# Kernel optimization log

Hardware: AMD Instinct MI355X
Metric: run time of the kernel (lower is better)

Reference implementation:

```python
import jax, jax.numpy as jnp
import numpy as np

S, M, B, D, H, DH = 1024, 1024, 4, 1024, 16, 64
T = S + M
EPS = 1e-5


def setup_inputs() -> dict:
    key = jax.random.key(0)
    ks = jax.random.split(key, 6)
    x = jax.random.normal(ks[0], (S, B, D), dtype=jnp.float32)
    pos_emb = jax.random.normal(ks[1], (S, 1, D), dtype=jnp.float32)
    memory = jax.random.normal(ks[2], (M, B, D), dtype=jnp.float32)
    # causal mask: query i (global position M+i) cannot attend to key j > M+i
    i = jnp.arange(S)[:, None]
    j = jnp.arange(T)[None, :]
    mask = jnp.broadcast_to((j > (i + M))[:, :, None], (S, T, B))  # [S,T,B] bool
    w_qkv = jax.random.normal(ks[3], (D, 3 * H * DH), dtype=jnp.float32) * (D ** -0.5)
    w_o = jax.random.normal(ks[4], (H * DH, D), dtype=jnp.float32) * ((H * DH) ** -0.5)
    ln_gamma = jnp.ones((D,), dtype=jnp.float32)
    ln_beta = jnp.zeros((D,), dtype=jnp.float32)
    return {"x": x, "pos_emb": pos_emb, "memory": memory, "mask": mask,
            "w_qkv": w_qkv, "w_o": w_o, "ln_gamma": ln_gamma, "ln_beta": ln_beta}


def reference(x, pos_emb, memory, mask, w_qkv, w_o, ln_gamma, ln_beta):
    seq_len = x.shape[0]
    scale = 1.0 / (DH ** 0.5)
    x = x + pos_emb[-seq_len:]                      # [S,B,D]
    c = jnp.concatenate([memory, x], axis=0)        # [T,B,D]
    qkv = jnp.einsum('tbd,de->tbe', c, w_qkv)       # [T,B,3*H*DH]
    q, k, v = jnp.split(qkv, 3, axis=-1)
    q = q.reshape(-1, B, H, DH)[-seq_len:]          # [S,B,H,DH]
    k = k.reshape(-1, B, H, DH)                     # [T,B,H,DH]
    v = v.reshape(-1, B, H, DH)
    score = jnp.einsum('ibnd,jbnd->ijbn', q, k) * scale  # [S,T,B,H]
    score = jnp.where(mask[:, :, :, None], -jnp.inf, score)
    prob = jax.nn.softmax(score, axis=1)
    vec = jnp.einsum('ijbn,jbnd->ibnd', prob, v)    # [S,B,H,DH]
    vec = vec.reshape(seq_len, B, H * DH)
    attn_out = jnp.einsum('sbe,ed->sbd', vec, w_o)  # [S,B,D]
    y = x + attn_out
    mu = jnp.mean(y, axis=-1, keepdims=True)
    var = jnp.mean(jnp.square(y - mu), axis=-1, keepdims=True)
    out = (y - mu) * jax.lax.rsqrt(var + EPS) * ln_gamma + ln_beta
    return out
```

## Files before the change

### kernel.cpp

```cpp
#include <hip/hip_runtime.h>
#include <stdint.h>

#define S_  1024
#define M_  1024
#define B_  4
#define D_  1024
#define H_  16
#define DH_ 64
#define T_  2048

typedef __attribute__((ext_vector_type(8))) short bf8;
typedef __attribute__((ext_vector_type(4))) float f32x4;
typedef __attribute__((ext_vector_type(16))) float f32x16;
typedef __attribute__((ext_vector_type(8))) unsigned short u16x8;
typedef __attribute__((ext_vector_type(4))) unsigned short u16x4;
typedef __attribute__((ext_vector_type(4))) unsigned int u32x4;
typedef unsigned short u16;

#define MFMA(a, b, c)   __builtin_amdgcn_mfma_f32_16x16x32_bf16((a), (b), (c), 0, 0, 0)
#define MFMA32(a, b, c) __builtin_amdgcn_mfma_f32_32x32x16_bf16((a), (b), (c), 0, 0, 0)

#define SIG(r) ((((r) >> 1) ^ ((r) >> 3)) & 3)

static __device__ __forceinline__ u16 f2bf(float f) {
  unsigned int u = __builtin_bit_cast(unsigned int, f);
  u += 0x7fffu + ((u >> 16) & 1u);
  return (u16)(u >> 16);
}

static __device__ __forceinline__ void gload16(const void* g, void* l) {
  __builtin_amdgcn_global_load_lds((const __attribute__((address_space(1))) unsigned int*)g,
                                   (__attribute__((address_space(3))) unsigned int*)l,
                                   16, 0, 0);
}

static __device__ __forceinline__ float fexp2(float x) {
  return __builtin_amdgcn_exp2f(x);
}
static __device__ __forceinline__ unsigned int cvtpk(float lo, float hi) {
  unsigned int r; asm("v_cvt_pk_bf16_f32 %0, %1, %2" : "=v"(r) : "v"(lo), "v"(hi)); return r;
}
static __device__ __forceinline__ void plswap(unsigned int& a, unsigned int& b) {
  asm volatile("s_nop 1\n\tv_permlane32_swap_b32 %0, %1" : "+v"(a), "+v"(b));
}

__global__ __launch_bounds__(256) void k_prep(const float* __restrict__ x,
    const float* __restrict__ pos, const float* __restrict__ mem,
    u16* __restrict__ cbf, float* __restrict__ xp)
{
  const int gid = blockIdx.x * 256 + threadIdx.x;
  const int e = gid * 8;
  const int row = e >> 10, col = e & 1023;
  float4 v0, v1;
  if (e < M_ * B_ * D_) {
    v0 = *(const float4*)(mem + e);
    v1 = *(const float4*)(mem + e + 4);
  } else {
    const int i2 = e - M_ * B_ * D_;
    v0 = *(const float4*)(x + i2);
    v1 = *(const float4*)(x + i2 + 4);
    const int srow = i2 >> 12;
    const float4 p0 = *(const float4*)(pos + srow * 1024 + col);
    const float4 p1 = *(const float4*)(pos + srow * 1024 + col + 4);
    v0.x += p0.x; v0.y += p0.y; v0.z += p0.z; v0.w += p0.w;
    v1.x += p1.x; v1.y += p1.y; v1.z += p1.z; v1.w += p1.w;
    *(float4*)(xp + i2) = v0;
    *(float4*)(xp + i2 + 4) = v1;
  }
  u16x8 c;
  c[0] = f2bf(v0.x); c[1] = f2bf(v0.y); c[2] = f2bf(v0.z); c[3] = f2bf(v0.w);
  c[4] = f2bf(v1.x); c[5] = f2bf(v1.y); c[6] = f2bf(v1.z); c[7] = f2bf(v1.w);
  const int ch = col >> 3;
  const int chs = (ch & ~3) | ((ch & 3) ^ SIG(row));
  *(u16x8*)(cbf + (size_t)row * 1024 + chs * 8) = c;
}

__global__ __launch_bounds__(256) void k_wtrans2(const float* __restrict__ wqkv,
    const float* __restrict__ wo, u16* __restrict__ wqt, u16* __restrict__ wot)
{
  __shared__ float tl[64][65];
  const int by = blockIdx.y;
  const float* src; u16* dst; int Cc, swz, c0;
  if (by < 48) { src = wqkv; dst = wqt; Cc = 3072; swz = 1; c0 = by * 64; }
  else         { src = wo;   dst = wot; Cc = 1024; swz = 0; c0 = (by - 48) * 64; }
  const int Rr = 1024;
  const int r0 = blockIdx.x * 64;
  const int tid = threadIdx.x;
  const int lr = tid >> 4, lc = (tid & 15) * 4;
  for (int i = 0; i < 4; ++i) {
    const int rr = lr + i * 16;
    const float4 v = *(const float4*)(src + (size_t)(r0 + rr) * Cc + c0 + lc);
    tl[rr][lc] = v.x; tl[rr][lc + 1] = v.y; tl[rr][lc + 2] = v.z; tl[rr][lc + 3] = v.w;
  }
  __syncthreads();
  const int c = tid >> 2, k0 = (tid & 3) * 16;
  u16x8 a, b;
  for (int j = 0; j < 8; ++j) { a[j] = f2bf(tl[k0 + j][c]); b[j] = f2bf(tl[k0 + 8 + j][c]); }
  const int roww = c0 + c;
  int ch0 = (r0 + k0) >> 3, ch1 = ((r0 + k0) >> 3) + 1;
  if (swz) {
    const int sx = SIG(roww);
    ch0 = (ch0 & ~3) | ((ch0 & 3) ^ sx);
    ch1 = (ch1 & ~3) | ((ch1 & 3) ^ sx);
  }
  u16* dp = dst + (size_t)roww * Rr;
  *(u16x8*)(dp + ch0 * 8) = a;
  *(u16x8*)(dp + ch1 * 8) = b;
}

__global__ __launch_bounds__(256, 3) void k_gemm_qkvs(const u16* __restrict__ A,
    const u16* __restrict__ Bt, u16* __restrict__ Qd, u16* __restrict__ Kd,
    u16* __restrict__ VTd)
{
  __shared__ u16 sA[3][4096];
  __shared__ u16 sB[3][4096];
  const int tid = threadIdx.x, lane = tid & 63, wave = tid >> 6;
  const int lrow = lane & 15, lgrp = lane >> 4;
  const int wm = (wave >> 1) * 64, wn = (wave & 1) * 64;
  const int sr = lane >> 2, sk = (lane & 3) * 8;

  const int bid = blockIdx.x;
  const int lid = (bid & 7) * 160 + (bid >> 3);
  int rowb, colb;
  if (lid < 512) { rowb = lid >> 4; colb = 8 + (lid & 15); }
  else { const int l2 = lid - 512; const int q = l2 / 24; rowb = 32 + q; colb = l2 - q * 24; }
  const int row0 = rowb * 128, col0 = colb * 128;

  f32x4 acc[4][4];
#pragma unroll
  for (int i = 0; i < 4; ++i)
#pragma unroll
    for (int j = 0; j < 4; ++j) acc[i][j] = f32x4{0.f, 0.f, 0.f, 0.f};

#define STAGE_S(bufi, kt) do { const int k0_ = (kt) * 32;                      \
    _Pragma("unroll") for (int s_ = 0; s_ < 2; ++s_) {                         \
      const int rr_ = (wave * 2 + s_) * 16 + sr;                               \
      gload16(A + (size_t)(row0 + rr_) * 1024 + k0_ + sk,                      \
              &sA[bufi][(wave * 2 + s_) * 512]);                               \
      gload16(Bt + (size_t)(col0 + rr_) * 1024 + k0_ + sk,                     \
              &sB[bufi][(wave * 2 + s_) * 512]);                               \
    } } while (0)

  STAGE_S(0, 0); STAGE_S(1, 1);

  int c0 = 0;
#pragma unroll 1
  for (int t = 0; t < 32; ++t) {
    if (t < 31) { asm volatile("s_waitcnt vmcnt(4)" ::: "memory"); }
    else        { asm volatile("s_waitcnt vmcnt(0)" ::: "memory"); }
    __builtin_amdgcn_s_barrier();
    __builtin_amdgcn_sched_barrier(0);
    const int c2 = (c0 + 2 >= 3) ? c0 - 1 : c0 + 2;
    if (t <= 29) STAGE_S(c2, t + 2);
    bf8 af[4], bfv[4];
#pragma unroll
    for (int i = 0; i < 4; ++i) {
      const int r_ = wm + i * 16 + lrow;
      af[i] = *(const bf8*)&sA[c0][r_ * 32 + ((lgrp ^ SIG(r_)) << 3)];
    }
#pragma unroll
    for (int j = 0; j < 4; ++j) {
      const int r_ = wn + j * 16 + lrow;
      bfv[j] = *(const bf8*)&sB[c0][r_ * 32 + ((lgrp ^ SIG(r_)) << 3)];
    }
    __builtin_amdgcn_s_setprio(1);
#pragma unroll
    for (int i = 0; i < 4; ++i)
#pragma unroll
      for (int j = 0; j < 4; ++j) acc[i][j] = MFMA(af[i], bfv[j], acc[i][j]);
    __builtin_amdgcn_s_setprio(0);
    c0 = (c0 == 2) ? 0 : c0 + 1;
  }

  const int which = col0 >> 10;
#pragma unroll
  for (int i = 0; i < 4; ++i)
#pragma unroll
    for (int j = 0; j < 4; ++j)
#pragma unroll
      for (int r = 0; r < 4; ++r) {
        const int grow = row0 + wm + i * 16 + lgrp * 4 + r;
        const int gcol = col0 + wn + j * 16 + lrow;
        const u16 bv = f2bf(acc[i][j][r]);
        const int t = grow >> 2, bb2 = grow & 3;
        const int rem = gcol & 1023;
        const int bh = bb2 * 16 + (rem >> 6), dh = rem & 63;
        if (which == 0) {
          if (t >= M_) Qd[((size_t)bh * S_ + (t - M_)) * 64 + dh] = bv;
        } else if (which == 1) {
          Kd[((size_t)bh * T_ + t) * 64 + (dh ^ ((t & 7) << 3))] = bv;
        } else {
          VTd[((size_t)bh * 64 + dh) * T_ + (t & ~63) + ((t & 63) ^ ((dh & 7) << 3))] = bv;
        }
      }
}

__global__ __launch_bounds__(256) void k_gemm_out(const u16* __restrict__ A,
    const u16* __restrict__ Bt, const float* __restrict__ xp,
    float* __restrict__ y)
{
  __shared__ u16 sA[3][2048];
  __shared__ u16 sB[3][4096];
  const int tid = threadIdx.x, lane = tid & 63, wave = tid >> 6;
  const int lrow = lane & 15, lgrp = lane >> 4;
  const int wm = (wave >> 1) * 32, wn = (wave & 1) * 64;
  const int row0 = blockIdx.y * 64, col0 = blockIdx.x * 128;
  const int sr = lane >> 2, sk = (lane & 3) * 8;

  f32x4 acc[2][4];
  for (int i = 0; i < 2; ++i)
    for (int j = 0; j < 4; ++j) acc[i][j] = f32x4{0.f, 0.f, 0.f, 0.f};

#define STAGE_O(bufi, kt) do { const int k0_ = (kt) * 32;                      \
    const int rra_ = wave * 16 + sr;                                           \
    gload16(A + (size_t)(row0 + rra_) * 1024 + k0_ + sk,                       \
            &sA[bufi][wave * 512]);                                            \
    _Pragma("unroll") for (int s_ = 0; s_ < 2; ++s_) {                         \
      const int rrb_ = (wave * 2 + s_) * 16 + sr;                              \
      gload16(Bt + (size_t)(col0 + rrb_) * 1024 + k0_ + sk,                    \
              &sB[bufi][(wave * 2 + s_) * 512]);                               \
    } } while (0)

  STAGE_O(0, 0); STAGE_O(1, 1);

  int c0 = 0;
#pragma unroll 1
  for (int kt = 0; kt < 32; ++kt) {
    if (kt < 31) { asm volatile("s_waitcnt vmcnt(3)" ::: "memory"); }
    else         { asm volatile("s_waitcnt vmcnt(0)" ::: "memory"); }
    __builtin_amdgcn_s_barrier();
    __builtin_amdgcn_sched_barrier(0);
    const int c2 = (c0 + 2 >= 3) ? c0 - 1 : c0 + 2;
    if (kt <= 29) STAGE_O(c2, kt + 2);
    bf8 af[2], bfv[4];
    const u16* pa = &sA[c0][(wm + lrow) * 32 + lgrp * 8];
    const u16* pb = &sB[c0][(wn + lrow) * 32 + lgrp * 8];
#pragma unroll
    for (int i = 0; i < 2; ++i) af[i] = *(const bf8*)(pa + i * 512);
#pragma unroll
    for (int j = 0; j < 4; ++j) bfv[j] = *(const bf8*)(pb + j * 512);
    __builtin_amdgcn_s_setprio(1);
#pragma unroll
    for (int i = 0; i < 2; ++i)
#pragma unroll
      for (int j = 0; j < 4; ++j) acc[i][j] = MFMA(af[i], bfv[j], acc[i][j]);
    __builtin_amdgcn_s_setprio(0);
    c0 = (c0 == 2) ? 0 : c0 + 1;
  }

  for (int i = 0; i < 2; ++i)
    for (int j = 0; j < 4; ++j)
      for (int r = 0; r < 4; ++r) {
        const int grow = row0 + wm + i * 16 + lgrp * 4 + r;
        const int gcol = col0 + wn + j * 16 + lrow;
        y[(size_t)grow * 1024 + gcol] = acc[i][j][r] + xp[(size_t)grow * 1024 + gcol];
      }
}

__global__ __launch_bounds__(256) void k_attn(const u16* __restrict__ Qd,
    const u16* __restrict__ Kd, const u16* __restrict__ VTd,
    u16* __restrict__ vec)
{
  __shared__ u16 Kl[2][4096];
  __shared__ u16 Vl[2][4096];
  const int tid = threadIdx.x, lane = tid & 63, wave = tid >> 6;
  const int ql = lane & 31, hi = lane >> 5;
  const int bid = blockIdx.x;
  const int sw = (bid & 7) * 64 + (bid >> 3);
  const int bh = sw >> 3, qb = sw & 7;
  const int bb = bh >> 4, hh = bh & 15;
  const int q0 = qb * 128 + wave * 32;
  const int myq = q0 + ql;
  const int klim = M_ + myq;

  bf8 qf[4];
  const u16* qrow = Qd + ((size_t)bh * S_ + myq) * 64 + hi * 8;
#pragma unroll
  for (int c = 0; c < 4; ++c) qf[c] = *(const bf8*)(qrow + c * 16);

  const u16* kb = Kd + (size_t)bh * T_ * 64;
  const u16* vb = VTd + (size_t)bh * 64 * T_;

  f32x16 o0, o1;
#pragma unroll
  for (int r = 0; r < 16; ++r) { o0[r] = 0.f; o1[r] = 0.f; }
  float m_run = 0.f, l_run = 0.f;
  const float cs = 0.125f * 1.44269504f;

  const int nkt = (M_ + qb * 128 + 128) >> 6;

  auto stage = [&](int buf, int kt) {
    const int t0 = kt * 64;
#pragma unroll
    for (int i = 0; i < 2; ++i) {
      const int ch = i * 256 + tid;
      gload16(kb + (size_t)t0 * 64 + ch * 8, &Kl[buf][ch * 8]);
    }
#pragma unroll
    for (int i = 0; i < 2; ++i) {
      const int ch = i * 256 + tid;
      gload16(vb + (size_t)(ch >> 3) * T_ + t0 + (ch & 7) * 8, &Vl[buf][ch * 8]);
    }
  };

  stage(0, 0);
  int cur = 0;
  for (int kt = 0; kt < nkt; ++kt) {
    if (kt + 1 < nkt) {
      stage(cur ^ 1, kt + 1);
      asm volatile("s_waitcnt vmcnt(4)" ::: "memory");
    } else {
      asm volatile("s_waitcnt vmcnt(0)" ::: "memory");
    }
    __builtin_amdgcn_s_barrier();

    const u16* Kc = Kl[cur];
    const u16* Vc = Vl[cur];

    f32x16 s0, s1;
#pragma unroll
    for (int r = 0; r < 16; ++r) { s0[r] = 0.f; s1[r] = 0.f; }
    const int tr0 = ql, tr1 = 32 + ql;
    const int sw0 = (tr0 & 7) << 3;
    __builtin_amdgcn_s_setprio(1);
#pragma unroll
    for (int c = 0; c < 4; ++c) {
      const int db = c * 16 + hi * 8;
      const bf8 ka = *(const bf8*)(Kc + tr0 * 64 + (db ^ sw0));
      const bf8 kbfr = *(const bf8*)(Kc + tr1 * 64 + (db ^ sw0));
      s0 = MFMA32(ka, qf[c], s0);
      s1 = MFMA32(kbfr, qf[c], s1);
    }
    __builtin_amdgcn_s_setprio(0);

    float p0[16], p1[16];
#pragma unroll
    for (int r = 0; r < 16; ++r) { p0[r] = s0[r] * cs; p1[r] = s1[r] * cs; }
    if (kt * 64 + 63 > M_ + q0) {
#pragma unroll
      for (int r = 0; r < 16; ++r) {
        const int kg = kt * 64 + (r & 3) + 8 * (r >> 2) + 4 * hi;
        if (kg > klim)      p0[r] = -1e30f;
        if (kg + 32 > klim) p1[r] = -1e30f;
      }
    }
    float mx = fmaxf(p0[0], p1[0]);
#pragma unroll
    for (int r = 1; r < 16; ++r) mx = fmaxf(mx, fmaxf(p0[r], p1[r]));
    mx = fmaxf(mx, __shfl_xor(mx, 32));
    if (__any(mx - m_run > 8.f)) {
      const float mnew = fmaxf(m_run, mx);
      const float al = fexp2(m_run - mnew);
      l_run *= al;
#pragma unroll
      for (int r = 0; r < 16; ++r) {
        const int qloc = (r & 3) + 8 * (r >> 2) + 4 * hi;
        const float ar = __shfl(al, (lane & 32) + qloc);
        o0[r] *= ar; o1[r] *= ar;
      }
      m_run = mnew;
    }
    float rs = 0.f;
#pragma unroll
    for (int r = 0; r < 16; ++r) {
      p0[r] = fexp2(p0[r] - m_run);
      p1[r] = fexp2(p1[r] - m_run);
      rs += p0[r] + p1[r];
    }
    rs += __shfl_xor(rs, 32);
    l_run += rs;

    bf8 paf[2][2];
    {
      unsigned int a0 = cvtpk(p0[0], p0[1]),  a1 = cvtpk(p0[2], p0[3]);
      unsigned int a2 = cvtpk(p0[4], p0[5]),  a3 = cvtpk(p0[6], p0[7]);
      unsigned int b0 = cvtpk(p0[8], p0[9]),  b1 = cvtpk(p0[10], p0[11]);
      unsigned int b2 = cvtpk(p0[12], p0[13]), b3 = cvtpk(p0[14], p0[15]);
      plswap(a0, a2); plswap(a1, a3); plswap(b0, b2); plswap(b1, b3);
      u32x4 f0 = {a0, a1, a2, a3}, f1 = {b0, b1, b2, b3};
      paf[0][0] = __builtin_bit_cast(bf8, f0);
      paf[0][1] = __builtin_bit_cast(bf8, f1);
    }
    {
      unsigned int a0 = cvtpk(p1[0], p1[1]),  a1 = cvtpk(p1[2], p1[3]);
      unsigned int a2 = cvtpk(p1[4], p1[5]),  a3 = cvtpk(p1[6], p1[7]);
      unsigned int b0 = cvtpk(p1[8], p1[9]),  b1 = cvtpk(p1[10], p1[11]);
      unsigned int b2 = cvtpk(p1[12], p1[13]), b3 = cvtpk(p1[14], p1[15]);
      plswap(a0, a2); plswap(a1, a3); plswap(b0, b2); plswap(b1, b3);
      u32x4 f0 = {a0, a1, a2, a3}, f1 = {b0, b1, b2, b3};
      paf[1][0] = __builtin_bit_cast(bf8, f0);
      paf[1][1] = __builtin_bit_cast(bf8, f1);
    }

    __builtin_amdgcn_s_setprio(1);
#pragma unroll
    for (int kc = 0; kc < 4; ++kc) {
      const int tb = kc * 16 + hi * 8;
      const bf8 pfrag = paf[kc >> 1][kc & 1];
      const int vr0 = ql, vr1 = 32 + ql;
      const bf8 vf0 = *(const bf8*)(Vc + vr0 * 64 + (tb ^ ((vr0 & 7) << 3)));
      const bf8 vf1 = *(const bf8*)(Vc + vr1 * 64 + (tb ^ ((vr1 & 7) << 3)));
      o0 = MFMA32(pfrag, vf0, o0);
      o1 = MFMA32(pfrag, vf1, o1);
    }
    __builtin_amdgcn_s_setprio(0);
    __builtin_amdgcn_s_barrier();
    cur ^= 1;
  }

  const float linv = 1.0f / l_run;
#pragma unroll
  for (int r = 0; r < 16; ++r) {
    const int qloc = (r & 3) + 8 * (r >> 2) + 4 * hi;
    const float li = __shfl(linv, (lane & 32) + qloc);
    const int srow = q0 + qloc;
    const size_t base = ((size_t)srow * B_ + bb) * 1024 + hh * 64;
    vec[base + ql]      = f2bf(o0[r] * li);
    vec[base + 32 + ql] = f2bf(o1[r] * li);
  }
}

__global__ __launch_bounds__(256) void k_ln(const float* __restrict__ y,
    const float* __restrict__ g, const float* __restrict__ be,
    float* __restrict__ out)
{
  const int row = blockIdx.x, tid = threadIdx.x;
  const float4 v = *(const float4*)(y + (size_t)row * 1024 + tid * 4);
  float s = v.x + v.y + v.z + v.w;
  float ss = v.x * v.x + v.y * v.y + v.z * v.z + v.w * v.w;
  for (int mk = 1; mk < 64; mk <<= 1) { s += __shfl_xor(s, mk); ss += __shfl_xor(ss, mk); }
  __shared__ float red[8];
  if ((tid & 63) == 0) { red[tid >> 6] = s; red[4 + (tid >> 6)] = ss; }
  __syncthreads();
  s = red[0] + red[1] + red[2] + red[3];
  ss = red[4] + red[5] + red[6] + red[7];
  const float mu = s * (1.0f / 1024.0f);
  const float var = ss * (1.0f / 1024.0f) - mu * mu;
  const float rstd = rsqrtf(var + 1e-5f);
  const float4 gg = *(const float4*)(g + tid * 4);
  const float4 bb = *(const float4*)(be + tid * 4);
  float4 o;
  o.x = (v.x - mu) * rstd * gg.x + bb.x;
  o.y = (v.y - mu) * rstd * gg.y + bb.y;
  o.z = (v.z - mu) * rstd * gg.z + bb.z;
  o.w = (v.w - mu) * rstd * gg.w + bb.w;
  *(float4*)(out + (size_t)row * 1024 + tid * 4) = o;
}

extern "C" void kernel_launch(void* const* d_in, const int* in_sizes, int n_in,
                              void* d_out, int out_size, void* d_ws, size_t ws_size,
                              hipStream_t stream)
{
  const float* x     = (const float*)d_in[0];
  const float* pos   = (const float*)d_in[1];
  const float* mem   = (const float*)d_in[2];
  const float* wqkv  = (const float*)d_in[4];
  const float* wo    = (const float*)d_in[5];
  const float* gamma = (const float*)d_in[6];
  const float* beta  = (const float*)d_in[7];
  float* out = (float*)d_out;

  if (ws_size < ((size_t)104 << 20)) return;

  char* ws = (char*)d_ws;
  u16*   cbf = (u16*)(ws + 0);
  float* y   = (float*)(ws + 0);
  float* xp  = (float*)(ws + ((size_t)16 << 20));
  u16*   wqt = (u16*)(ws + ((size_t)32 << 20));
  u16*   wot = (u16*)(ws + ((size_t)38 << 20));
  u16*   Qd  = (u16*)(ws + ((size_t)40 << 20));
  u16*   Kd  = (u16*)(ws + ((size_t)48 << 20));
  u16*   VTd = (u16*)(ws + ((size_t)80 << 20));
  u16*   vec = (u16*)(ws + ((size_t)96 << 20));

  k_prep<<<4096, 256, 0, stream>>>(x, pos, mem, cbf, xp);
  k_wtrans2<<<dim3(16, 64), 256, 0, stream>>>(wqkv, wo, wqt, wot);
  k_gemm_qkvs<<<1280, 256, 0, stream>>>(cbf, wqt, Qd, Kd, VTd);
  k_attn<<<512, 256, 0, stream>>>(Qd, Kd, VTd, vec);
  k_gemm_out<<<dim3(8, 64), 256, 0, stream>>>(vec, wot, xp, y);
  k_ln<<<4096, 256, 0, stream>>>(y, gamma, beta, out);
}
```

Before: 188.3 us.

## Rewrite QKV GEMM with 256x256 tiles, 8 waves, and phased ping-pong pipeline

Replaces the 128x128, 4-wave QKV projection GEMM with a 256x256 tile kernel using 512 threads and a K-step of 64. It double-buffers LDS and splits each step into phases that interleave LDS fragment loads, global prefetches and MFMA bursts with barriers and priority hints. The swizzle in the input conversion and weight transpose kernels moves from a 4-chunk signature to an 8-chunk XOR so the wider K rows can be read without bank conflicts. Larger tiles raise arithmetic intensity and cut global traffic, but they need more registers and LDS per block and launch only 320 blocks, so fewer blocks cover the GPU.

```diff
diff --git a/kernel.cpp b/kernel.cpp
--- a/kernel.cpp
+++ b/kernel.cpp
@@ -19,8 +19,6 @@
 
 #define MFMA(a, b, c)   __builtin_amdgcn_mfma_f32_16x16x32_bf16((a), (b), (c), 0, 0, 0)
 #define MFMA32(a, b, c) __builtin_amdgcn_mfma_f32_32x32x16_bf16((a), (b), (c), 0, 0, 0)
-
-#define SIG(r) ((((r) >> 1) ^ ((r) >> 3)) & 3)
 
 static __device__ __forceinline__ u16 f2bf(float f) {
   unsigned int u = __builtin_bit_cast(unsigned int, f);
@@ -71,7 +69,7 @@
   c[0] = f2bf(v0.x); c[1] = f2bf(v0.y); c[2] = f2bf(v0.z); c[3] = f2bf(v0.w);
   c[4] = f2bf(v1.x); c[5] = f2bf(v1.y); c[6] = f2bf(v1.z); c[7] = f2bf(v1.w);
   const int ch = col >> 3;
-  const int chs = (ch & ~3) | ((ch & 3) ^ SIG(row));
+  const int chs = (ch & ~7) | ((ch & 7) ^ (row & 7));
   *(u16x8*)(cbf + (size_t)row * 1024 + chs * 8) = c;
 }
 
@@ -99,100 +97,145 @@
   const int roww = c0 + c;
   int ch0 = (r0 + k0) >> 3, ch1 = ((r0 + k0) >> 3) + 1;
   if (swz) {
-    const int sx = SIG(roww);
-    ch0 = (ch0 & ~3) | ((ch0 & 3) ^ sx);
-    ch1 = (ch1 & ~3) | ((ch1 & 3) ^ sx);
+    const int sx = roww & 7;
+    ch0 = (ch0 & ~7) | ((ch0 & 7) ^ sx);
+    ch1 = (ch1 & ~7) | ((ch1 & 7) ^ sx);
   }
   u16* dp = dst + (size_t)roww * Rr;
   *(u16x8*)(dp + ch0 * 8) = a;
   *(u16x8*)(dp + ch1 * 8) = b;
 }
 
-__global__ __launch_bounds__(256, 3) void k_gemm_qkvs(const u16* __restrict__ A,
+__global__ __launch_bounds__(512, 2) void k_gemm_qkv8x(const u16* __restrict__ Aa,
     const u16* __restrict__ Bt, u16* __restrict__ Qd, u16* __restrict__ Kd,
     u16* __restrict__ VTd)
 {
-  __shared__ u16 sA[3][4096];
-  __shared__ u16 sB[3][4096];
+  __shared__ u16 lA[2][2][8192];
+  __shared__ u16 lB[2][2][8192];
   const int tid = threadIdx.x, lane = tid & 63, wave = tid >> 6;
   const int lrow = lane & 15, lgrp = lane >> 4;
-  const int wm = (wave >> 1) * 64, wn = (wave & 1) * 64;
-  const int sr = lane >> 2, sk = (lane & 3) * 8;
+  const int wr = wave >> 2, wc = wave & 3;
 
   const int bid = blockIdx.x;
-  const int lid = (bid & 7) * 160 + (bid >> 3);
+  const int lid = (bid & 7) * 40 + (bid >> 3);
   int rowb, colb;
-  if (lid < 512) { rowb = lid >> 4; colb = 8 + (lid & 15); }
-  else { const int l2 = lid - 512; const int q = l2 / 24; rowb = 32 + q; colb = l2 - q * 24; }
-  const int row0 = rowb * 128, col0 = colb * 128;
-
-  f32x4 acc[4][4];
-#pragma unroll
-  for (int i = 0; i < 4; ++i)
-#pragma unroll
-    for (int j = 0; j < 4; ++j) acc[i][j] = f32x4{0.f, 0.f, 0.f, 0.f};
-
-#define STAGE_S(bufi, kt) do { const int k0_ = (kt) * 32;                      \
+  if (lid < 256) { rowb = lid >> 3; colb = 4 + (lid & 7); }
+  else { const int l2 = lid - 256; rowb = 16 + (l2 >> 2); colb = l2 & 3; }
+  const int row0 = rowb * 256, col0 = colb * 256;
+
+  f32x4 acc[2][4][2][2];
+#pragma unroll
+  for (int a0 = 0; a0 < 2; ++a0)
+#pragma unroll
+    for (int a1 = 0; a1 < 4; ++a1)
+#pragma unroll
+      for (int a2 = 0; a2 < 2; ++a2)
+#pragma unroll
+        for (int a3 = 0; a3 < 2; ++a3)
+          acc[a0][a1][a2][a3] = f32x4{0.f, 0.f, 0.f, 0.f};
+
+  bf8 a_[4][2], b0_[2][2], b1_[2][2];
+
+#define STG_A(d, h, kt) do {                                                   \
     _Pragma("unroll") for (int s_ = 0; s_ < 2; ++s_) {                         \
-      const int rr_ = (wave * 2 + s_) * 16 + sr;                               \
-      gload16(A + (size_t)(row0 + rr_) * 1024 + k0_ + sk,                      \
-              &sA[bufi][(wave * 2 + s_) * 512]);                               \
-      gload16(Bt + (size_t)(col0 + rr_) * 1024 + k0_ + sk,                     \
-              &sB[bufi][(wave * 2 + s_) * 512]);                               \
+      const int c_ = s_ * 512 + tid;                                           \
+      const int row_ = c_ >> 3, kc_ = c_ & 7;                                  \
+      gload16(Aa + (size_t)(row0 + (h) * 128 + row_) * 1024 + (kt) * 64        \
+                   + kc_ * 8,                                                  \
+              &lA[d][h][(s_ * 512 + wave * 64) * 8]);                          \
     } } while (0)
 
-  STAGE_S(0, 0); STAGE_S(1, 1);
-
-  int c0 = 0;
+#define STG_B(d, h, kt) do {                                                   \
+    _Pragma("unroll") for (int s_ = 0; s_ < 2; ++s_) {                         \
+      const int c_ = s_ * 512 + tid;                                           \
+      const int row_ = c_ >> 3, kc_ = c_ & 7;                                  \
+      gload16(Bt + (size_t)(col0 + (h) * 128 + row_) * 1024 + (kt) * 64        \
+                   + kc_ * 8,                                                  \
+              &lB[d][h][(s_ * 512 + wave * 64) * 8]);                          \
+    } } while (0)
+
+#define LDA8(d, rh) do {                                                       \
+    _Pragma("unroll") for (int fi_ = 0; fi_ < 4; ++fi_)                        \
+    _Pragma("unroll") for (int ks_ = 0; ks_ < 2; ++ks_) {                      \
+      const int lr_ = (rh) * 64 + fi_ * 16 + lrow;                             \
+      a_[fi_][ks_] = *(const bf8*)&lA[d][wr][lr_ * 64                          \
+                         + (((ks_ * 4 + lgrp) ^ (lr_ & 7)) << 3)];             \
+    } } while (0)
+
+#define LDB4(d, ch, bq) do {                                                   \
+    _Pragma("unroll") for (int fj_ = 0; fj_ < 2; ++fj_)                        \
+    _Pragma("unroll") for (int ks_ = 0; ks_ < 2; ++ks_) {                      \
+      const int lc_ = (wc & 1) * 64 + (ch) * 32 + fj_ * 16 + lrow;             \
+      bq[fj_][ks_] = *(const bf8*)&lB[d][wc >> 1][lc_ * 64                     \
+                         + (((ks_ * 4 + lgrp) ^ (lc_ & 7)) << 3)];             \
+    } } while (0)
+
+#define MM16(rh, ch, bq) do {                                                  \
+    _Pragma("unroll") for (int fi_ = 0; fi_ < 4; ++fi_)                        \
+    _Pragma("unroll") for (int fj_ = 0; fj_ < 2; ++fj_)                        \
+    _Pragma("unroll") for (int ks_ = 0; ks_ < 2; ++ks_)                        \
+      acc[rh][fi_][ch][fj_] = MFMA(a_[fi_][ks_], bq[fj_][ks_],                 \
+                                   acc[rh][fi_][ch][fj_]);                     \
+  } while (0)
+
+#define PH_MID()  __builtin_amdgcn_s_barrier();                                \
+    asm volatile("s_waitcnt lgkmcnt(0)" ::: "memory");                         \
+    __builtin_amdgcn_sched_barrier(0);                                         \
+    __builtin_amdgcn_s_setprio(1)
+#define PH_CLOSE() __builtin_amdgcn_s_setprio(0);                              \
+    __builtin_amdgcn_sched_barrier(0);                                         \
+    __builtin_amdgcn_s_barrier()
+
+  STG_A(0, 0, 0); STG_A(0, 1, 0); STG_B(0, 0, 0); STG_B(0, 1, 0);
+  STG_A(1, 0, 1); STG_A(1, 1, 1); STG_B(1, 0, 1); STG_B(1, 1, 1);
+  asm volatile("s_waitcnt vmcnt(8)" ::: "memory");
+  __builtin_amdgcn_s_barrier();
+
 #pragma unroll 1
-  for (int t = 0; t < 32; ++t) {
-    if (t < 31) { asm volatile("s_waitcnt vmcnt(4)" ::: "memory"); }
-    else        { asm volatile("s_waitcnt vmcnt(0)" ::: "memory"); }
+  for (int t = 0; t < 16; ++t) {
+    const int d = t & 1;
+    LDA8(d, 0); LDB4(d, 0, b0_);
+    PH_MID(); MM16(0, 0, b0_); PH_CLOSE();
+    LDB4(d, 1, b1_);
+    PH_MID(); MM16(0, 1, b1_); PH_CLOSE();
+    LDA8(d, 1);
+    if (t < 14) { STG_B(d, 0, t + 2); STG_B(d, 1, t + 2); }
+    PH_MID(); MM16(1, 1, b1_); PH_CLOSE();
+    if (t < 14) { STG_A(d, 0, t + 2); STG_A(d, 1, t + 2); }
+    __builtin_amdgcn_s_setprio(1);
+    MM16(1, 0, b0_);
+    __builtin_amdgcn_s_setprio(0);
+    __builtin_amdgcn_sched_barrier(0);
+    if (t < 14)       { asm volatile("s_waitcnt vmcnt(8)" ::: "memory"); }
+    else if (t == 14) { asm volatile("s_waitcnt vmcnt(0)" ::: "memory"); }
     __builtin_amdgcn_s_barrier();
-    __builtin_amdgcn_sched_barrier(0);
-    const int c2 = (c0 + 2 >= 3) ? c0 - 1 : c0 + 2;
-    if (t <= 29) STAGE_S(c2, t + 2);
-    bf8 af[4], bfv[4];
-#pragma unroll
-    for (int i = 0; i < 4; ++i) {
-      const int r_ = wm + i * 16 + lrow;
-      af[i] = *(const bf8*)&sA[c0][r_ * 32 + ((lgrp ^ SIG(r_)) << 3)];
-    }
-#pragma unroll
-    for (int j = 0; j < 4; ++j) {
-      const int r_ = wn + j * 16 + lrow;
-      bfv[j] = *(const bf8*)&sB[c0][r_ * 32 + ((lgrp ^ SIG(r_)) << 3)];
-    }
-    __builtin_amdgcn_s_setprio(1);
-#pragma unroll
-    for (int i = 0; i < 4; ++i)
-#pragma unroll
-      for (int j = 0; j < 4; ++j) acc[i][j] = MFMA(af[i], bfv[j], acc[i][j]);
-    __builtin_amdgcn_s_setprio(0);
-    c0 = (c0 == 2) ? 0 : c0 + 1;
   }
 
   const int which = col0 >> 10;
 #pragma unroll
-  for (int i = 0; i < 4; ++i)
-#pragma unroll
-    for (int j = 0; j < 4; ++j)
-#pragma unroll
-      for (int r = 0; r < 4; ++r) {
-        const int grow = row0 + wm + i * 16 + lgrp * 4 + r;
-        const int gcol = col0 + wn + j * 16 + lrow;
-        const u16 bv = f2bf(acc[i][j][r]);
-        const int t = grow >> 2, bb2 = grow & 3;
-        const int rem = gcol & 1023;
-        const int bh = bb2 * 16 + (rem >> 6), dh = rem & 63;
-        if (which == 0) {
-          if (t >= M_) Qd[((size_t)bh * S_ + (t - M_)) * 64 + dh] = bv;
-        } else if (which == 1) {
-          Kd[((size_t)bh * T_ + t) * 64 + (dh ^ ((t & 7) << 3))] = bv;
-        } else {
-          VTd[((size_t)bh * 64 + dh) * T_ + (t & ~63) + ((t & 63) ^ ((dh & 7) << 3))] = bv;
-        }
-      }
+  for (int rh = 0; rh < 2; ++rh)
+#pragma unroll
+    for (int fi = 0; fi < 4; ++fi)
+#pragma unroll
+      for (int ch = 0; ch < 2; ++ch)
+#pragma unroll
+        for (int fj = 0; fj < 2; ++fj)
+#pragma unroll
+          for (int r = 0; r < 4; ++r) {
+            const int grow = row0 + wr * 128 + rh * 64 + fi * 16 + lgrp * 4 + r;
+            const int gcol = col0 + wc * 64 + ch * 32 + fj * 16 + lrow;
+            const u16 bv = f2bf(acc[rh][fi][ch][fj][r]);
+            const int t = grow >> 2, bb2 = grow & 3;
+            const int rem = gcol & 1023;
+            const int bh = bb2 * 16 + (rem >> 6), dh = rem & 63;
+            if (which == 0) {
+              if (t >= M_) Qd[((size_t)bh * S_ + (t - M_)) * 64 + dh] = bv;
+            } else if (which == 1) {
+              Kd[((size_t)bh * T_ + t) * 64 + (dh ^ ((t & 7) << 3))] = bv;
+            } else {
+              VTd[((size_t)bh * 64 + dh) * T_ + (t & ~63) + ((t & 63) ^ ((dh & 7) << 3))] = bv;
+            }
+          }
 }
 
 __global__ __launch_bounds__(256) void k_gemm_out(const u16* __restrict__ A,
@@ -475,7 +518,7 @@
 
   k_prep<<<4096, 256, 0, stream>>>(x, pos, mem, cbf, xp);
   k_wtrans2<<<dim3(16, 64), 256, 0, stream>>>(wqkv, wo, wqt, wot);
-  k_gemm_qkvs<<<1280, 256, 0, stream>>>(cbf, wqt, Qd, Kd, VTd);
+  k_gemm_qkv8x<<<320, 512, 0, stream>>>(cbf, wqt, Qd, Kd, VTd);
   k_attn<<<512, 256, 0, stream>>>(Qd, Kd, VTd, vec);
   k_gemm_out<<<dim3(8, 64), 256, 0, stream>>>(vec, wot, xp, y);
   k_ln<<<4096, 256, 0, stream>>>(y, gamma, beta, out);
```

Measured after the change: 211.4 us. +12.3%, slower.
